# Kernel optimization log

Hardware: AMD Instinct MI355X
Metric: run time of the kernel (lower is better)

Reference implementation:

```python
import jax, jax.numpy as jnp
import numpy as np
from jax import lax

EPS = 1e-5
B, T, I, H = 524288, 6, 4, 20


def batchnorm1d(x, gamma, beta):
    # x: [B, C, L]; training-mode BatchNorm1d over (batch, L) per channel C,
    # biased variance, matching torch's normalization in train().
    mean = jnp.mean(x, axis=(0, 2), keepdims=True)
    var = jnp.mean(jnp.square(x - mean), axis=(0, 2), keepdims=True)
    xhat = (x - mean) * lax.rsqrt(var + EPS)
    return xhat * gamma[None, :, None] + beta[None, :, None]


def lstm_layer(x, W_ih, W_hh, b_ih, b_hh):
    # x: [B, T, in]; torch gate order i, f, g, o; returns h sequence [B, T, H]
    Bsz = x.shape[0]
    Hd = W_hh.shape[1]
    # precompute input contribution for all steps: [B, T, 4H]
    xg = jnp.einsum('bti,gi->btg', x, W_ih) + b_ih + b_hh

    def step(carry, xg_t):
        h, c = carry
        g = xg_t + h @ W_hh.T  # [B, 4H]
        i, f, gg, o = jnp.split(g, 4, axis=-1)
        i = jax.nn.sigmoid(i)
        f = jax.nn.sigmoid(f)
        gg = jnp.tanh(gg)
        o = jax.nn.sigmoid(o)
        c = f * c + i * gg
        h = o * jnp.tanh(c)
        return (h, c), h

    h0 = jnp.zeros((Bsz, Hd), x.dtype)
    c0 = jnp.zeros((Bsz, Hd), x.dtype)
    _, hs = lax.scan(step, (h0, c0), jnp.swapaxes(xg, 0, 1))  # [T, B, H]
    return jnp.swapaxes(hs, 0, 1)


def setup_inputs() -> dict:
    key = jax.random.key(0)
    ks = jax.random.split(key, 12)
    s_ih0 = 1.0 / np.sqrt(H)
    d = {
        'x': jax.random.normal(ks[0], (B, T, I), jnp.float32),
        'gamma': jnp.ones((T,), jnp.float32),
        'beta': jnp.zeros((T,), jnp.float32),
        'W_ih0': jax.random.uniform(ks[1], (4 * H, I), jnp.float32, -s_ih0, s_ih0),
        'W_hh0': jax.random.uniform(ks[2], (4 * H, H), jnp.float32, -s_ih0, s_ih0),
        'b_ih0': jax.random.uniform(ks[3], (4 * H,), jnp.float32, -s_ih0, s_ih0),
        'b_hh0': jax.random.uniform(ks[4], (4 * H,), jnp.float32, -s_ih0, s_ih0),
        'W_ih1': jax.random.uniform(ks[5], (4 * H, H), jnp.float32, -s_ih0, s_ih0),
        'W_hh1': jax.random.uniform(ks[6], (4 * H, H), jnp.float32, -s_ih0, s_ih0),
        'b_ih1': jax.random.uniform(ks[7], (4 * H,), jnp.float32, -s_ih0, s_ih0),
        'b_hh1': jax.random.uniform(ks[8], (4 * H,), jnp.float32, -s_ih0, s_ih0),
        'W_out': jax.random.uniform(ks[9], (1, H), jnp.float32, -s_ih0, s_ih0),
        'b_out': jax.random.uniform(ks[10], (1,), jnp.float32, -s_ih0, s_ih0),
    }
    return d


def reference(x, gamma, beta, W_ih0, W_hh0, b_ih0, b_hh0,
              W_ih1, W_hh1, b_ih1, b_hh1, W_out, b_out):
    # bn over time-channel axis (C = TIME_STEP = 6)
    x = batchnorm1d(x, gamma, beta)                # [B, 6, 4]
    h1 = lstm_layer(x, W_ih0, W_hh0, b_ih0, b_hh0)  # [B, 6, 20]
    h2 = lstm_layer(h1, W_ih1, W_hh1, b_ih1, b_hh1)  # [B, 6, 20]
    r = batchnorm1d(h2, gamma, beta)               # same shared bn module
    out = r[:, -1, :] @ W_out.T + b_out            # [B, 1]
    return out
```

## Files before the change

### kernel.cpp

```cpp
#include <hip/hip_runtime.h>

#define EPS 1e-5f
#define BATCH 524288
#define BLK 256
#define RBLK 1024
#define NPREP 60
#define NBLK2 4096
#define NBLKO 2048

typedef float f32x4 __attribute__((ext_vector_type(4)));
typedef __bf16 bf16x8 __attribute__((ext_vector_type(8)));

#define AF_A0    0
#define AF_A1K0  5120
#define AF_A1K1  10240
#define AF_TOT   15360
#define OFF_ACC  7680

__device__ __forceinline__ float sigm(float x) {
    return __builtin_amdgcn_rcpf(1.0f + __expf(-x));
}
__device__ __forceinline__ float tanh_f(float x) {
    return 1.0f - 2.0f * __builtin_amdgcn_rcpf(1.0f + __expf(2.0f * x));
}
__device__ __forceinline__ float wave_reduce(float v) {
    #pragma unroll
    for (int o = 32; o; o >>= 1) v += __shfl_down(v, o, 64);
    return v;
}

struct HiLo { bf16x8 hi, lo; };
__device__ __forceinline__ HiLo cvt8(f32x4 a, f32x4 b) {
    HiLo r;
    #pragma unroll
    for (int i = 0; i < 4; ++i) {
        float v = a[i];
        __bf16 h = (__bf16)v;
        r.hi[i] = h; r.lo[i] = (__bf16)(v - (float)h);
        float w = b[i];
        __bf16 h2 = (__bf16)w;
        r.hi[4 + i] = h2; r.lo[4 + i] = (__bf16)(w - (float)h2);
    }
    return r;
}
#define MFMA16(C_, A_, B_) \
    (C_) = __builtin_amdgcn_mfma_f32_16x16x32_bf16((A_), (B_), (C_), 0, 0, 0)

__global__ __launch_bounds__(BLK) void k_prep(
    const float* __restrict__ Wih0, const float* __restrict__ Whh0,
    const float* __restrict__ bih0, const float* __restrict__ bhh0,
    const float* __restrict__ Wih1, const float* __restrict__ Whh1,
    const float* __restrict__ bih1, const float* __restrict__ bhh1,
    float* __restrict__ ws) {
    int gtid = blockIdx.x * BLK + threadIdx.x;
    unsigned short* af = (unsigned short*)ws;
    if (gtid < AF_TOT) {
        int idx = gtid;
        float w = 0.f; int s;
        if (idx < AF_A1K0) {
            int e = idx, fid = e >> 9; e &= 511;
            int l = e >> 3, i = e & 7;
            int tm = fid >> 1; s = fid & 1;
            int q = l >> 4, m = l & 15;
            int wrow = (m & 3) * 20 + 4 * tm + (m >> 2);
            int k = 4 * q + (i & 3) + 16 * (i >> 2);
            w = (k < 20) ? Whh0[wrow * 20 + k]
              : (k < 24) ? Wih0[wrow * 4 + (k - 20)]
              : (k == 24) ? (bih0[wrow] + bhh0[wrow]) : 0.f;
        } else if (idx < AF_A1K1) {
            int e = idx - AF_A1K0, fid = e >> 9; e &= 511;
            int l = e >> 3, i = e & 7;
            int tm = fid >> 1; s = fid & 1;
            int q = l >> 4, m = l & 15;
            int wrow = (m & 3) * 20 + 4 * tm + (m >> 2);
            int k = 4 * q + (i & 3) + 16 * (i >> 2);
            w = (k < 20) ? Wih1[wrow * 20 + k] : Whh1[wrow * 20 + (k - 20)];
        } else {
            int e = idx - AF_A1K1, fid = e >> 9; e &= 511;
            int l = e >> 3, i = e & 7;
            int tm = fid >> 1; s = fid & 1;
            int q = l >> 4, m = l & 15;
            int wrow = (m & 3) * 20 + 4 * tm + (m >> 2);
            w = (q < 2 && i < 4) ? Whh1[wrow * 20 + 12 + 4 * q + i]
              : (q == 2 && i == 0) ? (bih1[wrow] + bhh1[wrow]) : 0.f;
        }
        float fh = (float)(__bf16)w;
        float v = s ? (w - fh) : w;
        af[idx] = __builtin_bit_cast(unsigned short, (__bf16)v);
    }
    if (gtid < 16) ws[OFF_ACC + gtid] = 0.f;
}

__global__ __launch_bounds__(BLK) void k_reduce_x(const float* __restrict__ x,
                                                  float* __restrict__ acc) {
    float s[6], q[6];
    #pragma unroll
    for (int t = 0; t < 6; ++t) { s[t] = 0.f; q[t] = 0.f; }
    for (int b = blockIdx.x * BLK + threadIdx.x; b < BATCH; b += RBLK * BLK) {
        const float4* xp = (const float4*)(x + (size_t)b * 24);
        #pragma unroll
        for (int t = 0; t < 6; ++t) {
            float4 v = xp[t];
            s[t] += (v.x + v.y) + (v.z + v.w);
            q[t] += (v.x * v.x + v.y * v.y) + (v.z * v.z + v.w * v.w);
        }
    }
    __shared__ float red[4 * 12];
    int wid = threadIdx.x >> 6, lane = threadIdx.x & 63;
    #pragma unroll
    for (int c = 0; c < 6; ++c) {
        float rs = wave_reduce(s[c]);
        float rq = wave_reduce(q[c]);
        if (lane == 0) { red[wid * 12 + c] = rs; red[wid * 12 + 6 + c] = rq; }
    }
    __syncthreads();
    if (threadIdx.x < 12) {
        float tot = red[threadIdx.x] + red[12 + threadIdx.x] +
                    red[24 + threadIdx.x] + red[36 + threadIdx.x];
        atomicAdd(&acc[threadIdx.x], tot);
    }
}

__global__ __launch_bounds__(BLK, 1) void k_lstm(
    const float* __restrict__ x,
    const float* __restrict__ wsT,
    const float* __restrict__ gamma, const float* __restrict__ beta,
    const float* __restrict__ Wout,
    float* __restrict__ dotout, float* __restrict__ acc2) {
    __shared__ __align__(16) float sBounce[4 * 1408];

    const int tid = threadIdx.x;
    const int wid = tid >> 6, lane = tid & 63;
    const int q = lane >> 4, col = lane & 15;
    const int wb = blockIdx.x * 128 + wid * 32;
    float* buf = sBounce + wid * 1408;
    float* bc0 = buf + col * 44;
    float* bc1 = bc0 + 16 * 44;

    const unsigned short* af = (const unsigned short*)wsT;
    bf16x8 A0h[5], A0l[5], A1h[5], A1l[5], A2h[5], A2l[5];
    #pragma unroll
    for (int tm = 0; tm < 5; ++tm) {
        A0h[tm] = *(const bf16x8*)(af + AF_A0   + (2 * tm) * 512 + lane * 8);
        A0l[tm] = *(const bf16x8*)(af + AF_A0   + (2 * tm + 1) * 512 + lane * 8);
        A1h[tm] = *(const bf16x8*)(af + AF_A1K0 + (2 * tm) * 512 + lane * 8);
        A1l[tm] = *(const bf16x8*)(af + AF_A1K0 + (2 * tm + 1) * 512 + lane * 8);
        A2h[tm] = *(const bf16x8*)(af + AF_A1K1 + (2 * tm) * 512 + lane * 8);
        A2l[tm] = *(const bf16x8*)(af + AF_A1K1 + (2 * tm + 1) * 512 + lane * 8);
    }
    const float* accp = wsT + OFF_ACC;

    for (int m = lane; m < 1408; m += 64) buf[m] = 0.f;

    float c0s[5][2], c1s[5][2];
    #pragma unroll
    for (int tm = 0; tm < 5; ++tm)
        #pragma unroll
        for (int nt = 0; nt < 2; ++nt) { c0s[tm][nt] = 0.f; c1s[tm][nt] = 0.f; }

    const float* xb0 = x + (size_t)(wb + col) * 24 + q;
    const float* xb1 = x + (size_t)(wb + 16 + col) * 24 + q;
    float x0c = xb0[0], x1c = xb1[0];

    #pragma unroll 1
    for (int t = 0; t < 6; ++t) {
        const float invN = 1.0f / ((float)BATCH * 4.0f);
        float mean = accp[t] * invN;
        float var = accp[6 + t] * invN - mean * mean;
        float inv = rsqrtf(var + EPS);
        float at = gamma[t] * inv;
        float bt = beta[t] - mean * at;

        float x0n = 0.f, x1n = 0.f;
        if (t < 5) { x0n = xb0[(t + 1) * 4]; x1n = xb1[(t + 1) * 4]; }
        bc0[40 + q] = fmaf(at, x0c, bt);
        bc1[40 + q] = fmaf(at, x1c, bt);

        HiLo b0[2];
        #pragma unroll
        for (int nt = 0; nt < 2; ++nt) {
            const float* bp = nt ? bc1 : bc0;
            f32x4 va = *(const f32x4*)(bp + 4 * q);
            f32x4 vb = {0.f, 0.f, 0.f, 0.f};
            if (q < 2) vb = *(const f32x4*)(bp + (q ? 40 : 16));
            else if (q == 2) vb[0] = 1.0f;
            b0[nt] = cvt8(va, vb);
        }
        #pragma unroll
        for (int tm = 0; tm < 5; ++tm) {
            #pragma unroll
            for (int nt = 0; nt < 2; ++nt) {
                f32x4 c = {0.f, 0.f, 0.f, 0.f};
                MFMA16(c, A0h[tm], b0[nt].hi);
                MFMA16(c, A0h[tm], b0[nt].lo);
                MFMA16(c, A0l[tm], b0[nt].hi);
                float ii = sigm(c[0]), ff = sigm(c[1]);
                float gg = tanh_f(c[2]), oo = sigm(c[3]);
                float cn = fmaf(ff, c0s[tm][nt], ii * gg);
                c0s[tm][nt] = cn;
                (nt ? bc1 : bc0)[4 * tm + q] = oo * tanh_f(cn);
            }
        }

        HiLo b1[2], b2[2];
        #pragma unroll
        for (int nt = 0; nt < 2; ++nt) {
            const float* bp = nt ? bc1 : bc0;
            f32x4 va = *(const f32x4*)(bp + 4 * q);
            f32x4 vb = *(const f32x4*)(bp + 16 + 4 * q);
            b1[nt] = cvt8(va, vb);
            f32x4 vc = {0.f, 0.f, 0.f, 0.f};
            if (q < 2) vc = *(const f32x4*)(bp + 32 + 4 * q);
            else if (q == 2) vc[0] = 1.0f;
            f32x4 vz = {0.f, 0.f, 0.f, 0.f};
            b2[nt] = cvt8(vc, vz);
        }
        #pragma unroll
        for (int tm = 0; tm < 5; ++tm) {
            #pragma unroll
            for (int nt = 0; nt < 2; ++nt) {
                f32x4 c = {0.f, 0.f, 0.f, 0.f};
                MFMA16(c, A1h[tm], b1[nt].hi);
                MFMA16(c, A1h[tm], b1[nt].lo);
                MFMA16(c, A1l[tm], b1[nt].hi);
                MFMA16(c, A2h[tm], b2[nt].hi);
                MFMA16(c, A2h[tm], b2[nt].lo);
                MFMA16(c, A2l[tm], b2[nt].hi);
                float ii = sigm(c[0]), ff = sigm(c[1]);
                float gg = tanh_f(c[2]), oo = sigm(c[3]);
                float cn = fmaf(ff, c1s[tm][nt], ii * gg);
                c1s[tm][nt] = cn;
                (nt ? bc1 : bc0)[20 + 4 * tm + q] = oo * tanh_f(cn);
            }
        }
        x0c = x0n; x1c = x1n;
    }

    float wout[5];
    #pragma unroll
    for (int tm = 0; tm < 5; ++tm) wout[tm] = Wout[4 * tm + q];
    float psum = 0.f, psq = 0.f;
    float dsum[2];
    #pragma unroll
    for (int nt = 0; nt < 2; ++nt) {
        const float* bp = nt ? bc1 : bc0;
        float d = 0.f;
        #pragma unroll
        for (int tm = 0; tm < 5; ++tm) {
            float v = bp[20 + 4 * tm + q];
            d = fmaf(v, wout[tm], d);
            psum += v; psq = fmaf(v, v, psq);
        }
        d += __shfl_xor(d, 16);
        d += __shfl_xor(d, 32);
        dsum[nt] = d;
    }
    if (q == 0) {
        dotout[wb + col] = dsum[0];
        dotout[wb + 16 + col] = dsum[1];
    }
    psum = wave_reduce(psum);
    psq = wave_reduce(psq);
    __syncthreads();
    if (lane == 0) { sBounce[wid] = psum; sBounce[4 + wid] = psq; }
    __syncthreads();
    if (tid == 0) {
        atomicAdd(&acc2[0], sBounce[0] + sBounce[1] + sBounce[2] + sBounce[3]);
        atomicAdd(&acc2[1], sBounce[4] + sBounce[5] + sBounce[6] + sBounce[7]);
    }
}

__global__ __launch_bounds__(BLK) void k_out(float* __restrict__ out,
                                             const float* __restrict__ ws,
                                             const float* __restrict__ gamma,
                                             const float* __restrict__ beta,
                                             const float* __restrict__ Wout,
                                             const float* __restrict__ bout) {
    float S = ws[OFF_ACC + 12], Q = ws[OFF_ACC + 13];
    const float N = (float)BATCH * 20.0f;
    float m = S / N, var = Q / N - m * m;
    float s1 = gamma[5] * rsqrtf(var + EPS);
    float sw = 0.f;
    #pragma unroll
    for (int h = 0; h < 20; ++h) sw += Wout[h];
    float s2 = (beta[5] - m * s1) * sw + bout[0];
    int i = blockIdx.x * BLK + threadIdx.x;
    out[i] = s1 * out[i] + s2;
}

extern "C" void kernel_launch(void* const* d_in, const int* in_sizes, int n_in,
                              void* d_out, int out_size, void* d_ws, size_t ws_size,
                              hipStream_t stream) {
    const float* x     = (const float*)d_in[0];
    const float* gamma = (const float*)d_in[1];
    const float* beta  = (const float*)d_in[2];
    const float* Wih0  = (const float*)d_in[3];
    const float* Whh0  = (const float*)d_in[4];
    const float* bih0  = (const float*)d_in[5];
    const float* bhh0  = (const float*)d_in[6];
    const float* Wih1  = (const float*)d_in[7];
    const float* Whh1  = (const float*)d_in[8];
    const float* bih1  = (const float*)d_in[9];
    const float* bhh1  = (const float*)d_in[10];
    const float* Wout  = (const float*)d_in[11];
    const float* bout  = (const float*)d_in[12];
    float* out = (float*)d_out;
    float* ws = (float*)d_ws;

    k_prep<<<NPREP, BLK, 0, stream>>>(Wih0, Whh0, bih0, bhh0,
                                      Wih1, Whh1, bih1, bhh1, ws);
    k_reduce_x<<<RBLK, BLK, 0, stream>>>(x, ws + OFF_ACC);
    k_lstm<<<NBLK2, BLK, 0, stream>>>(x, ws, gamma, beta, Wout,
                                      out, ws + OFF_ACC + 12);
    k_out<<<NBLKO, BLK, 0, stream>>>(out, ws, gamma, beta, Wout, bout);
}
```

Baseline: 334.3 us.

## Stage LSTM weights in LDS, fold activation scales, spread atomics

The LSTM kernel no longer keeps all weight fragments in registers. It stages them in shared memory and reloads them per tile, and the launch bound rises from 1 to 3 blocks per SM for more occupancy. The sigmoid/tanh input scales (-log2e, 2log2e) are folded into the weights at prep time so activations use exp2 directly. Atomic accumulators are padded to separate cache lines, and the second-stage sum is spread across 16 slots to cut atomic contention. The reduce grid shrinks and batchnorm coefficients are computed once per step ahead of use. Possible costs are added LDS traffic per MFMA and a larger LDS footprint, which may limit the occupancy gain.

Result: slower. 352.3 us (+5.4%).

```diff
diff --git a/kernel.cpp b/kernel.cpp
--- a/kernel.cpp
+++ b/kernel.cpp
@@ -3,7 +3,7 @@
 #define EPS 1e-5f
 #define BATCH 524288
 #define BLK 256
-#define RBLK 1024
+#define RBLK 256
 #define NPREP 60
 #define NBLK2 4096
 #define NBLKO 2048
@@ -16,13 +16,12 @@
 #define AF_A1K1  10240
 #define AF_TOT   15360
 #define OFF_ACC  7680
-
-__device__ __forceinline__ float sigm(float x) {
-    return __builtin_amdgcn_rcpf(1.0f + __expf(-x));
-}
-__device__ __forceinline__ float tanh_f(float x) {
-    return 1.0f - 2.0f * __builtin_amdgcn_rcpf(1.0f + __expf(2.0f * x));
-}
+#define OFF_AC2  7872
+#define NZERO    704
+
+#define SCL_SIG  (-1.4426950409f)
+#define SCL_TANH (2.8853900817f)
+
 __device__ __forceinline__ float wave_reduce(float v) {
     #pragma unroll
     for (int o = 32; o; o >>= 1) v += __shfl_down(v, o, 64);
@@ -45,6 +44,18 @@
 }
 #define MFMA16(C_, A_, B_) \
     (C_) = __builtin_amdgcn_mfma_f32_16x16x32_bf16((A_), (B_), (C_), 0, 0, 0)
+
+#define GATEACT(C_, CS_, DST_) do {                                        \
+    float ii = __builtin_amdgcn_rcpf(1.0f + exp2f((C_)[0]));               \
+    float ff = __builtin_amdgcn_rcpf(1.0f + exp2f((C_)[1]));               \
+    float gg = 1.0f - 2.0f * __builtin_amdgcn_rcpf(1.0f + exp2f((C_)[2])); \
+    float oo = __builtin_amdgcn_rcpf(1.0f + exp2f((C_)[3]));               \
+    float cn = fmaf(ff, (CS_), ii * gg);                                   \
+    (CS_) = cn;                                                            \
+    float th = 1.0f - 2.0f * __builtin_amdgcn_rcpf(                        \
+                   1.0f + exp2f(cn * SCL_TANH));                           \
+    (DST_) = oo * th;                                                      \
+} while (0)
 
 __global__ __launch_bounds__(BLK) void k_prep(
     const float* __restrict__ Wih0, const float* __restrict__ Whh0,
@@ -57,12 +68,14 @@
     if (gtid < AF_TOT) {
         int idx = gtid;
         float w = 0.f; int s;
+        int gate;
         if (idx < AF_A1K0) {
             int e = idx, fid = e >> 9; e &= 511;
             int l = e >> 3, i = e & 7;
             int tm = fid >> 1; s = fid & 1;
             int q = l >> 4, m = l & 15;
-            int wrow = (m & 3) * 20 + 4 * tm + (m >> 2);
+            gate = m & 3;
+            int wrow = gate * 20 + 4 * tm + (m >> 2);
             int k = 4 * q + (i & 3) + 16 * (i >> 2);
             w = (k < 20) ? Whh0[wrow * 20 + k]
               : (k < 24) ? Wih0[wrow * 4 + (k - 20)]
@@ -72,7 +85,8 @@
             int l = e >> 3, i = e & 7;
             int tm = fid >> 1; s = fid & 1;
             int q = l >> 4, m = l & 15;
-            int wrow = (m & 3) * 20 + 4 * tm + (m >> 2);
+            gate = m & 3;
+            int wrow = gate * 20 + 4 * tm + (m >> 2);
             int k = 4 * q + (i & 3) + 16 * (i >> 2);
             w = (k < 20) ? Wih1[wrow * 20 + k] : Whh1[wrow * 20 + (k - 20)];
         } else {
@@ -80,15 +94,17 @@
             int l = e >> 3, i = e & 7;
             int tm = fid >> 1; s = fid & 1;
             int q = l >> 4, m = l & 15;
-            int wrow = (m & 3) * 20 + 4 * tm + (m >> 2);
+            gate = m & 3;
+            int wrow = gate * 20 + 4 * tm + (m >> 2);
             w = (q < 2 && i < 4) ? Whh1[wrow * 20 + 12 + 4 * q + i]
               : (q == 2 && i == 0) ? (bih1[wrow] + bhh1[wrow]) : 0.f;
         }
+        w *= (gate == 2) ? SCL_TANH : SCL_SIG;
         float fh = (float)(__bf16)w;
         float v = s ? (w - fh) : w;
         af[idx] = __builtin_bit_cast(unsigned short, (__bf16)v);
     }
-    if (gtid < 16) ws[OFF_ACC + gtid] = 0.f;
+    if (gtid < NZERO) ws[OFF_ACC + gtid] = 0.f;
 }
 
 __global__ __launch_bounds__(BLK) void k_reduce_x(const float* __restrict__ x,
@@ -117,16 +133,17 @@
     if (threadIdx.x < 12) {
         float tot = red[threadIdx.x] + red[12 + threadIdx.x] +
                     red[24 + threadIdx.x] + red[36 + threadIdx.x];
-        atomicAdd(&acc[threadIdx.x], tot);
-    }
-}
-
-__global__ __launch_bounds__(BLK, 1) void k_lstm(
+        atomicAdd(&acc[threadIdx.x * 16], tot);
+    }
+}
+
+__global__ __launch_bounds__(BLK, 3) void k_lstm(
     const float* __restrict__ x,
     const float* __restrict__ wsT,
     const float* __restrict__ gamma, const float* __restrict__ beta,
     const float* __restrict__ Wout,
     float* __restrict__ dotout, float* __restrict__ acc2) {
+    __shared__ __align__(16) unsigned short sAF[AF_TOT];
     __shared__ __align__(16) float sBounce[4 * 1408];
 
     const int tid = threadIdx.x;
@@ -137,16 +154,10 @@
     float* bc0 = buf + col * 44;
     float* bc1 = bc0 + 16 * 44;
 
-    const unsigned short* af = (const unsigned short*)wsT;
-    bf16x8 A0h[5], A0l[5], A1h[5], A1l[5], A2h[5], A2l[5];
-    #pragma unroll
-    for (int tm = 0; tm < 5; ++tm) {
-        A0h[tm] = *(const bf16x8*)(af + AF_A0   + (2 * tm) * 512 + lane * 8);
-        A0l[tm] = *(const bf16x8*)(af + AF_A0   + (2 * tm + 1) * 512 + lane * 8);
-        A1h[tm] = *(const bf16x8*)(af + AF_A1K0 + (2 * tm) * 512 + lane * 8);
-        A1l[tm] = *(const bf16x8*)(af + AF_A1K0 + (2 * tm + 1) * 512 + lane * 8);
-        A2h[tm] = *(const bf16x8*)(af + AF_A1K1 + (2 * tm) * 512 + lane * 8);
-        A2l[tm] = *(const bf16x8*)(af + AF_A1K1 + (2 * tm + 1) * 512 + lane * 8);
+    {
+        const uint4* src = (const uint4*)wsT;
+        uint4* dst = (uint4*)sAF;
+        for (int m = tid; m < AF_TOT / 8; m += BLK) dst[m] = src[m];
     }
     const float* accp = wsT + OFF_ACC;
 
@@ -160,21 +171,26 @@
 
     const float* xb0 = x + (size_t)(wb + col) * 24 + q;
     const float* xb1 = x + (size_t)(wb + 16 + col) * 24 + q;
-    float x0c = xb0[0], x1c = xb1[0];
+
+    const float invN = 1.0f / ((float)BATCH * 4.0f);
+    {
+        float mean = accp[0] * invN;
+        float var = accp[6 * 16] * invN - mean * mean;
+        float a0 = gamma[0] * rsqrtf(var + EPS);
+        float b0v = beta[0] - mean * a0;
+        bc0[40 + q] = fmaf(a0, xb0[0], b0v);
+        bc1[40 + q] = fmaf(a0, xb1[0], b0v);
+    }
+    __syncthreads();
 
     #pragma unroll 1
     for (int t = 0; t < 6; ++t) {
-        const float invN = 1.0f / ((float)BATCH * 4.0f);
-        float mean = accp[t] * invN;
-        float var = accp[6 + t] * invN - mean * mean;
-        float inv = rsqrtf(var + EPS);
-        float at = gamma[t] * inv;
-        float bt = beta[t] - mean * at;
+        int zo = 0;
+        asm volatile("" : "+s"(zo));
+        const unsigned short* AF = sAF + zo;
 
         float x0n = 0.f, x1n = 0.f;
         if (t < 5) { x0n = xb0[(t + 1) * 4]; x1n = xb1[(t + 1) * 4]; }
-        bc0[40 + q] = fmaf(at, x0c, bt);
-        bc1[40 + q] = fmaf(at, x1c, bt);
 
         HiLo b0[2];
         #pragma unroll
@@ -187,18 +203,19 @@
             b0[nt] = cvt8(va, vb);
         }
         #pragma unroll
-        for (int tm = 0; tm < 5; ++tm) {
+        for (int tmi = 0; tmi < 5; ++tmi) {
+            const int tm = (tmi == 0) ? 4 : (tmi - 1);
+            bf16x8 ahi = *(const bf16x8*)(AF + AF_A0 + (2 * tm) * 512 + lane * 8);
+            bf16x8 alo = *(const bf16x8*)(AF + AF_A0 + (2 * tm + 1) * 512 + lane * 8);
             #pragma unroll
             for (int nt = 0; nt < 2; ++nt) {
                 f32x4 c = {0.f, 0.f, 0.f, 0.f};
-                MFMA16(c, A0h[tm], b0[nt].hi);
-                MFMA16(c, A0h[tm], b0[nt].lo);
-                MFMA16(c, A0l[tm], b0[nt].hi);
-                float ii = sigm(c[0]), ff = sigm(c[1]);
-                float gg = tanh_f(c[2]), oo = sigm(c[3]);
-                float cn = fmaf(ff, c0s[tm][nt], ii * gg);
-                c0s[tm][nt] = cn;
-                (nt ? bc1 : bc0)[4 * tm + q] = oo * tanh_f(cn);
+                MFMA16(c, ahi, b0[nt].hi);
+                MFMA16(c, ahi, b0[nt].lo);
+                MFMA16(c, alo, b0[nt].hi);
+                float h;
+                GATEACT(c, c0s[tm][nt], h);
+                (nt ? bc1 : bc0)[4 * tm + q] = h;
             }
         }
 
@@ -215,25 +232,36 @@
             f32x4 vz = {0.f, 0.f, 0.f, 0.f};
             b2[nt] = cvt8(vc, vz);
         }
+
+        if (t < 5) {
+            float mean = accp[(t + 1) * 16] * invN;
+            float var = accp[(6 + t + 1) * 16] * invN - mean * mean;
+            float at = gamma[t + 1] * rsqrtf(var + EPS);
+            float bt = beta[t + 1] - mean * at;
+            bc0[40 + q] = fmaf(at, x0n, bt);
+            bc1[40 + q] = fmaf(at, x1n, bt);
+        }
+
         #pragma unroll
         for (int tm = 0; tm < 5; ++tm) {
+            bf16x8 ahi0 = *(const bf16x8*)(AF + AF_A1K0 + (2 * tm) * 512 + lane * 8);
+            bf16x8 alo0 = *(const bf16x8*)(AF + AF_A1K0 + (2 * tm + 1) * 512 + lane * 8);
+            bf16x8 ahi1 = *(const bf16x8*)(AF + AF_A1K1 + (2 * tm) * 512 + lane * 8);
+            bf16x8 alo1 = *(const bf16x8*)(AF + AF_A1K1 + (2 * tm + 1) * 512 + lane * 8);
             #pragma unroll
             for (int nt = 0; nt < 2; ++nt) {
                 f32x4 c = {0.f, 0.f, 0.f, 0.f};
-                MFMA16(c, A1h[tm], b1[nt].hi);
-                MFMA16(c, A1h[tm], b1[nt].lo);
-                MFMA16(c, A1l[tm], b1[nt].hi);
-                MFMA16(c, A2h[tm], b2[nt].hi);
-                MFMA16(c, A2h[tm], b2[nt].lo);
-                MFMA16(c, A2l[tm], b2[nt].hi);
-                float ii = sigm(c[0]), ff = sigm(c[1]);
-                float gg = tanh_f(c[2]), oo = sigm(c[3]);
-                float cn = fmaf(ff, c1s[tm][nt], ii * gg);
-                c1s[tm][nt] = cn;
-                (nt ? bc1 : bc0)[20 + 4 * tm + q] = oo * tanh_f(cn);
+                MFMA16(c, ahi0, b1[nt].hi);
+                MFMA16(c, ahi0, b1[nt].lo);
+                MFMA16(c, alo0, b1[nt].hi);
+                MFMA16(c, ahi1, b2[nt].hi);
+                MFMA16(c, ahi1, b2[nt].lo);
+                MFMA16(c, alo1, b2[nt].hi);
+                float h;
+                GATEACT(c, c1s[tm][nt], h);
+                (nt ? bc1 : bc0)[20 + 4 * tm + q] = h;
             }
         }
-        x0c = x0n; x1c = x1n;
     }
 
     float wout[5];
@@ -265,8 +293,11 @@
     if (lane == 0) { sBounce[wid] = psum; sBounce[4 + wid] = psq; }
     __syncthreads();
     if (tid == 0) {
-        atomicAdd(&acc2[0], sBounce[0] + sBounce[1] + sBounce[2] + sBounce[3]);
-        atomicAdd(&acc2[1], sBounce[4] + sBounce[5] + sBounce[6] + sBounce[7]);
+        int slot = blockIdx.x & 15;
+        atomicAdd(&acc2[slot * 16],
+                  sBounce[0] + sBounce[1] + sBounce[2] + sBounce[3]);
+        atomicAdd(&acc2[(16 + slot) * 16],
+                  sBounce[4] + sBounce[5] + sBounce[6] + sBounce[7]);
     }
 }
 
@@ -276,7 +307,12 @@
                                              const float* __restrict__ beta,
                                              const float* __restrict__ Wout,
                                              const float* __restrict__ bout) {
-    float S = ws[OFF_ACC + 12], Q = ws[OFF_ACC + 13];
+    float S = 0.f, Q = 0.f;
+    #pragma unroll
+    for (int s = 0; s < 16; ++s) {
+        S += ws[OFF_AC2 + s * 16];
+        Q += ws[OFF_AC2 + (16 + s) * 16];
+    }
     const float N = (float)BATCH * 20.0f;
     float m = S / N, var = Q / N - m * m;
     float s1 = gamma[5] * rsqrtf(var + EPS);
@@ -311,6 +347,6 @@
                                       Wih1, Whh1, bih1, bhh1, ws);
     k_reduce_x<<<RBLK, BLK, 0, stream>>>(x, ws + OFF_ACC);
     k_lstm<<<NBLK2, BLK, 0, stream>>>(x, ws, gamma, beta, Wout,
-                                      out, ws + OFF_ACC + 12);
+                                      out, ws + OFF_AC2);
     k_out<<<NBLKO, BLK, 0, stream>>>(out, ws, gamma, beta, Wout, bout);
 }
```
